# Performance work log

Measured on AMD Instinct MI355X. Metric: run time of the kernel, lower is better.

## Reference

```python
import jax, jax.numpy as jnp
import numpy as np
from jax import lax

B, CIN, COUT, H, W, K = 256, 512, 256, 8, 8, 8192


def setup_inputs() -> dict:
    key = jax.random.key(0)
    ks = jax.random.split(key, 6)
    scale = 0.05
    return {
        "latent": jax.random.normal(ks[0], (B, CIN, H, W), dtype=jnp.float32),
        "conv_w": jax.random.normal(ks[1], (COUT, CIN, 3, 3), dtype=jnp.float32) * scale,
        "conv_b": jax.random.normal(ks[2], (COUT,), dtype=jnp.float32) * scale,
        "lin_w": jax.random.normal(ks[3], (COUT, COUT), dtype=jnp.float32) * scale,
        "lin_b": jax.random.normal(ks[4], (COUT,), dtype=jnp.float32) * scale,
        "emb": jax.random.normal(ks[5], (K, COUT), dtype=jnp.float32),
    }


def reference(latent, conv_w, conv_b, lin_w, lin_b, emb):
    # pre-quantization conv: 3x3, stride 1, padding 1 (SAME), NCHW / OIHW
    x = lax.conv_general_dilated(
        latent, conv_w, window_strides=(1, 1), padding="SAME",
        dimension_numbers=("NCHW", "OIHW", "NCHW"),
    ) + conv_b[None, :, None, None]
    # permute(0,2,3,1) then linear on last dim
    x = jnp.transpose(x, (0, 2, 3, 1))              # [B,H,W,C]
    x = jnp.einsum("bhwc,dc->bhwd", x, lin_w) + lin_b
    flat = x.reshape(-1, x.shape[-1])               # [B*H*W, C]
    distances = (
        jnp.sum(flat ** 2, axis=1, keepdims=True)
        + jnp.sum(emb ** 2, axis=1)
        - 2.0 * flat @ emb.T
    )                                               # [B*H*W, K]
    encoding_indices = jnp.argmin(distances, axis=1)
    return encoding_indices.reshape(-1, 64)
```

## Files before the change

### kernel.cpp

```cpp
#include <hip/hip_runtime.h>
#include <cstdint>
#include <cstddef>


#define CIN_  512
#define E_    4608
#define M_    16384

typedef _Float16 half4_t __attribute__((ext_vector_type(4)));
typedef _Float16 half8_t __attribute__((ext_vector_type(8)));
typedef float f32x4 __attribute__((ext_vector_type(4)));

#define GLOAD_LDS16(gptr, lptr)                                         \
    __builtin_amdgcn_global_load_lds(                                   \
        (const __attribute__((address_space(1))) unsigned int*)(gptr),  \
        (__attribute__((address_space(3))) unsigned int*)(lptr), 16, 0, 0)

__global__ void tkern(const float* __restrict__ src, float* __restrict__ dst,
                      int R, int C) {
    __shared__ float t[32][33];
    int c = blockIdx.x * 32 + threadIdx.x;
    int r = blockIdx.y * 32 + threadIdx.y;
    if (r < R && c < C) t[threadIdx.y][threadIdx.x] = src[(size_t)r * C + c];
    __syncthreads();
    int rr = blockIdx.x * 32 + threadIdx.y;
    int cc = blockIdx.y * 32 + threadIdx.x;
    if (rr < C && cc < R) dst[(size_t)rr * R + cc] = t[threadIdx.x][threadIdx.y];
}

__global__ __launch_bounds__(256) void fold5_k(const float* __restrict__ conv_w,
                                               const float* __restrict__ lwT,
                                               _Float16* __restrict__ W2x) {
    int e0 = blockIdx.x * 8;
    int d = threadIdx.x;
    float acc[8];
    #pragma unroll
    for (int j = 0; j < 8; ++j) acc[j] = 0.f;
    for (int co = 0; co < 256; ++co) {
        float lw = lwT[co * 256 + d];
        const float* cwr = conv_w + (size_t)co * E_ + e0;
        #pragma unroll
        for (int j = 0; j < 8; ++j) acc[j] += cwr[j] * lw;
    }
    #pragma unroll
    for (int j = 0; j < 8; ++j) {
        int e = e0 + j;
        int c = e / 9, t9 = e - c * 9;
        _Float16 h = (_Float16)acc[j];
        _Float16 l = (_Float16)(acc[j] - (float)h);
        W2x[((size_t)(t9 * 256 + d)) * 512 + c] = h;
        W2x[((size_t)((9 + t9) * 256 + d)) * 512 + c] = l;
    }
}

__global__ void bias_k(const float* __restrict__ lwT, const float* __restrict__ conv_b,
                       const float* __restrict__ lin_b, float* __restrict__ b2) {
    int d = threadIdx.x;
    float acc = lin_b[d];
    for (int co = 0; co < 256; ++co) acc += lwT[co * 256 + d] * conv_b[co];
    b2[d] = acc;
}

__global__ __launch_bounds__(256) void packlat_k(const float* __restrict__ lat,
                                                 _Float16* __restrict__ Xnp) {
    int b = blockIdx.x, t = threadIdx.x;
    __shared__ float lt[128][65];
    const float* src = lat + (size_t)b * 512 * 64;
    _Float16* dst = Xnp + (size_t)b * 64 * 1024;
    for (int c0 = 0; c0 < 512; c0 += 128) {
        __syncthreads();
        #pragma unroll
        for (int j = 0; j < 8; ++j) {
            int f4 = t + j * 256;
            int cc = f4 >> 4, p4 = (f4 & 15) * 4;
            float4 v = *(const float4*)(src + (size_t)(c0 + cc) * 64 + p4);
            lt[cc][p4] = v.x; lt[cc][p4 + 1] = v.y;
            lt[cc][p4 + 2] = v.z; lt[cc][p4 + 3] = v.w;
        }
        __syncthreads();
        int pix = t >> 2, cr = (t & 3) * 32;
        #pragma unroll
        for (int q = 0; q < 4; ++q) {
            half8_t hh, ll;
            #pragma unroll
            for (int j = 0; j < 8; ++j) {
                float v = lt[cr + q * 8 + j][pix];
                _Float16 h = (_Float16)v;
                hh[j] = h; ll[j] = (_Float16)(v - (float)h);
            }
            *(half8_t*)(dst + (size_t)pix * 1024 + c0 + cr + q * 8) = hh;
            *(half8_t*)(dst + (size_t)pix * 1024 + 512 + c0 + cr + q * 8) = ll;
        }
    }
}

__global__ __launch_bounds__(256) void convm6_k(
    const _Float16* __restrict__ Xnp, const _Float16* __restrict__ W2x,
    const float* __restrict__ b2, float* __restrict__ yb) {
    __shared__ char sm[65536];
    int m0 = blockIdx.x * 128, n0 = blockIdx.y * 128;
    int tid = threadIdx.x, w = tid >> 6, lane = tid & 63;
    int wm = w & 1, wn = w >> 1;
    int fr = lane & 15, fq = lane >> 4;

    int xq = (fq ^ ((fr >> 1) & 3)) << 4;
    int boff[4];
    #pragma unroll
    for (int i = 0; i < 4; ++i) boff[i] = (wn * 64 + i * 16 + fr) * 64 + xq;
    int imgoff[4], ph[4], pw[4];
    #pragma unroll
    for (int s = 0; s < 4; ++s) {
        int rr = wm * 64 + s * 16 + fr;
        imgoff[s] = rr & 64; ph[s] = (rr >> 3) & 7; pw[s] = rr & 7;
    }
    int slt[2], sr[2], sq[2];
    #pragma unroll
    for (int i = 0; i < 2; ++i) {
        int s = w * 128 + i * 64 + lane;
        slt[i] = s;
        sr[i] = s >> 2;
        sq[i] = ((s & 3) ^ ((s >> 3) & 3)) * 8;
    }

    auto stageA = [&](int cc, int buf) {
        char* L = sm + buf * 16384;
        #pragma unroll
        for (int i = 0; i < 2; ++i) {
            const _Float16* base =
                Xnp + (size_t)(m0 + sr[i]) * 1024 + cc * 32 + sq[i];
            GLOAD_LDS16(base, L + slt[i] * 16);
            GLOAD_LDS16(base + 512, L + 8192 + slt[i] * 16);
        }
    };
    auto stageB = [&](int tap, int cc, int buf) {
        char* L = sm + 32768 + buf * 16384;
        #pragma unroll
        for (int i = 0; i < 2; ++i) {
            const _Float16* bb =
                W2x + ((size_t)(tap * 256 + n0 + sr[i])) * 512 + cc * 32 + sq[i];
            GLOAD_LDS16(bb, L + slt[i] * 16);
            GLOAD_LDS16(bb + (size_t)9 * 256 * 512, L + 8192 + slt[i] * 16);
        }
    };

    f32x4 acc[4][4];
    #pragma unroll
    for (int s = 0; s < 4; ++s)
        #pragma unroll
        for (int t = 0; t < 4; ++t)
            #pragma unroll
            for (int r = 0; r < 4; ++r) acc[s][t][r] = 0.f;

    stageA(0, 0);
    stageB(0, 0, 0);
    const half8_t zfrag = {};
    int gi = 0;
    for (int cc = 0; cc < 16; ++cc) {
        const char* Ab = sm + (cc & 1) * 16384;
        for (int tap = 0; tap < 9; ++tap, ++gi) {
            __syncthreads();
            if (tap < 8) stageB(tap + 1, cc, (gi + 1) & 1);
            else if (cc < 15) stageB(0, cc + 1, (gi + 1) & 1);
            if (tap == 7 && cc < 15) stageA(cc + 1, (cc + 1) & 1);

            int dy = tap / 3 - 1, dx = tap - (tap / 3) * 3 - 1;
            half8_t ah[4], al[4];
            #pragma unroll
            for (int s = 0; s < 4; ++s) {
                int ih = ph[s] + dy, iw = pw[s] + dx;
                bool v = ((unsigned)ih < 8u) && ((unsigned)iw < 8u);
                int pp = imgoff[s] + (v ? ih * 8 + iw : 0);
                int ao = pp * 64 + ((fq ^ ((pp >> 1) & 3)) << 4);
                half8_t a0 = *(const half8_t*)(Ab + ao);
                half8_t a1 = *(const half8_t*)(Ab + 8192 + ao);
                ah[s] = v ? a0 : zfrag;
                al[s] = v ? a1 : zfrag;
            }
            const char* Bb = sm + 32768 + (gi & 1) * 16384;
            half8_t bh[4], bl[4];
            #pragma unroll
            for (int t = 0; t < 4; ++t) {
                bh[t] = *(const half8_t*)(Bb + boff[t]);
                bl[t] = *(const half8_t*)(Bb + 8192 + boff[t]);
            }
            #pragma unroll
            for (int s = 0; s < 4; ++s)
                #pragma unroll
                for (int t = 0; t < 4; ++t)
                    acc[s][t] = __builtin_amdgcn_mfma_f32_16x16x32_f16(
                        ah[s], bh[t], acc[s][t], 0, 0, 0);
            #pragma unroll
            for (int s = 0; s < 4; ++s)
                #pragma unroll
                for (int t = 0; t < 4; ++t)
                    acc[s][t] = __builtin_amdgcn_mfma_f32_16x16x32_f16(
                        ah[s], bl[t], acc[s][t], 0, 0, 0);
            #pragma unroll
            for (int s = 0; s < 4; ++s)
                #pragma unroll
                for (int t = 0; t < 4; ++t)
                    acc[s][t] = __builtin_amdgcn_mfma_f32_16x16x32_f16(
                        al[s], bh[t], acc[s][t], 0, 0, 0);
        }
    }

    float bv[4];
    #pragma unroll
    for (int t = 0; t < 4; ++t) bv[t] = b2[n0 + wn * 64 + t * 16 + fr];
    #pragma unroll
    for (int s = 0; s < 4; ++s)
        #pragma unroll
        for (int r = 0; r < 4; ++r) {
            int m = m0 + wm * 64 + s * 16 + fq * 4 + r;
            #pragma unroll
            for (int t = 0; t < 4; ++t) {
                int d = n0 + wn * 64 + t * 16 + fr;
                yb[(size_t)m * 256 + d] = acc[s][t][r] + bv[t];
            }
        }
}

__global__ __launch_bounds__(256) void pack2_k(
    const float* __restrict__ yb, const float* __restrict__ emb,
    _Float16* __restrict__ A2, _Float16* __restrict__ B2,
    float* __restrict__ esq) {
    #pragma unroll
    for (int it = 0; it < 8; ++it) {
        int i = (blockIdx.x + it * 512) * 256 + threadIdx.x;
        float4 v = *(const float4*)(yb + (size_t)i * 4);
        half4_t h = {(_Float16)v.x, (_Float16)v.y, (_Float16)v.z, (_Float16)v.w};
        *(half4_t*)(A2 + (size_t)i * 4) = h;
    }
    int w = threadIdx.x >> 6, lane = threadIdx.x & 63;
    #pragma unroll
    for (int j = 0; j < 4; ++j) {
        int k = blockIdx.x * 16 + w * 4 + j;
        float4 v = *(const float4*)(emb + (size_t)k * 256 + lane * 4);
        half4_t h = {(_Float16)v.x, (_Float16)v.y, (_Float16)v.z, (_Float16)v.w};
        *(half4_t*)(B2 + (size_t)k * 256 + lane * 4) = h;
        float s = v.x * v.x + v.y * v.y + v.z * v.z + v.w * v.w;
        #pragma unroll
        for (int m = 32; m >= 1; m >>= 1) s += __shfl_xor(s, m, 64);
        if (lane == 0) esq[k] = s;
    }
}

__global__ __launch_bounds__(512) void screen11_k(
    const _Float16* __restrict__ A2, const _Float16* __restrict__ B2,
    const float* __restrict__ esq, float* __restrict__ ps2, int* __restrict__ pi2) {
    __shared__ char sm[49152];
    int Lb = blockIdx.x;
    int xcd = Lb & 7, j = Lb >> 3;
    int mt = xcd * 16 + (j & 15);
    int nt = j >> 4;
    int m0 = mt * 128, n0 = nt * 256;
    int tid = threadIdx.x, w = tid >> 6, lane = tid & 63;
    int wm = w & 1, wn = w >> 1;
    int fr = lane & 15, fq = lane >> 4;

    int xq = (fq ^ ((fr >> 1) & 3)) << 4;
    int aoff[4], boff[4];
    #pragma unroll
    for (int i = 0; i < 4; ++i) {
        aoff[i] = (wm * 64 + i * 16 + fr) * 64 + xq;
        boff[i] = (wn * 64 + i * 16 + fr) * 64 + xq;
    }
    int sAr = tid >> 2, sAq = ((tid & 3) ^ ((tid >> 3) & 3)) * 8;
    int sBs[2], sBr[2], sBq[2];
    #pragma unroll
    for (int i = 0; i < 2; ++i) {
        int s = i * 512 + tid;
        sBs[i] = s;
        sBr[i] = s >> 2;
        sBq[i] = ((s & 3) ^ ((s >> 3) & 3)) * 8;
    }

    auto stage = [&](int kt, int buf) {
        char* L = sm + buf * 24576;
        int ko = kt * 32;
        GLOAD_LDS16(A2 + (size_t)(m0 + sAr) * 256 + ko + sAq, L + tid * 16);
        #pragma unroll
        for (int i = 0; i < 2; ++i)
            GLOAD_LDS16(B2 + (size_t)(n0 + sBr[i]) * 256 + ko + sBq[i],
                        L + 8192 + sBs[i] * 16);
    };

    f32x4 acc[4][4];
    #pragma unroll
    for (int s = 0; s < 4; ++s)
        #pragma unroll
        for (int t = 0; t < 4; ++t)
            #pragma unroll
            for (int r = 0; r < 4; ++r) acc[s][t][r] = 0.f;

    stage(0, 0);
    for (int kt = 0; kt < 8; ++kt) {
        __syncthreads();
        if (kt + 1 < 8) stage(kt + 1, (kt + 1) & 1);
        const char* L = sm + (kt & 1) * 24576;
        half8_t af[4], bf[4];
        #pragma unroll
        for (int s = 0; s < 4; ++s) af[s] = *(const half8_t*)(L + aoff[s]);
        #pragma unroll
        for (int t = 0; t < 4; ++t) bf[t] = *(const half8_t*)(L + 8192 + boff[t]);
        #pragma unroll
        for (int s = 0; s < 4; ++s)
            #pragma unroll
            for (int t = 0; t < 4; ++t)
                acc[s][t] = __builtin_amdgcn_mfma_f32_16x16x32_f16(
                    af[s], bf[t], acc[s][t], 0, 0, 0);
    }

    float esv[4];
    #pragma unroll
    for (int t = 0; t < 4; ++t) esv[t] = esq[n0 + wn * 64 + t * 16 + fr];
    int colIdx = nt * 4 + wn;
    #pragma unroll
    for (int s = 0; s < 4; ++s) {
        #pragma unroll
        for (int r = 0; r < 4; ++r) {
            float best = 3.4e38f; int bidx = 0x7fffffff;
            #pragma unroll
            for (int t = 0; t < 4; ++t) {
                float sc = esv[t] - 2.f * acc[s][t][r];
                int k = n0 + wn * 64 + t * 16 + fr;
                if (sc < best || (sc == best && k < bidx)) { best = sc; bidx = k; }
            }
            #pragma unroll
            for (int msk = 1; msk <= 8; msk <<= 1) {
                float so = __shfl_xor(best, msk, 64);
                int ko2 = __shfl_xor(bidx, msk, 64);
                if (so < best || (so == best && ko2 < bidx)) { best = so; bidx = ko2; }
            }
            if (fr == 0) {
                int m = m0 + wm * 64 + s * 16 + fq * 4 + r;
                ps2[(size_t)m * 128 + colIdx] = best;
                pi2[(size_t)m * 128 + colIdx] = bidx;
            }
        }
    }
}

__global__ __launch_bounds__(256) void refine3_k(
    const float* __restrict__ y, const float* __restrict__ emb,
    const float* __restrict__ esq, const float* __restrict__ ps2,
    const int* __restrict__ pi2, int* __restrict__ out) {
    int lane = threadIdx.x & 63;
    for (int j = 0; j < 8; ++j) {
        int m = blockIdx.x * 32 + j * 4 + (threadIdx.x >> 6);
        float4 yv = *(const float4*)(y + (size_t)m * 256 + lane * 4);
        float sc_[2]; int kc_[2];
        #pragma unroll
        for (int i = 0; i < 2; ++i) {
            sc_[i] = ps2[(size_t)m * 128 + lane * 2 + i];
            kc_[i] = pi2[(size_t)m * 128 + lane * 2 + i];
        }
        float s0 = fminf(sc_[0], sc_[1]);
        #pragma unroll
        for (int msk = 1; msk <= 32; msk <<= 1) s0 = fminf(s0, __shfl_xor(s0, msk, 64));
        float thr = s0 + 0.25f;
        float best = 3.4e38f; int bk = 0x7fffffff;
        for (int c = 0; c < 128; ++c) {
            float scc = __shfl(sc_[c & 1], c >> 1, 64);
            if (scc <= thr) {
                int k = __shfl(kc_[c & 1], c >> 1, 64);
                float4 ev = *(const float4*)(emb + (size_t)k * 256 + lane * 4);
                float d = yv.x * ev.x + yv.y * ev.y + yv.z * ev.z + yv.w * ev.w;
                #pragma unroll
                for (int msk = 1; msk <= 32; msk <<= 1) d += __shfl_xor(d, msk, 64);
                float sx = esq[k] - 2.f * d;
                if (sx < best || (sx == best && k < bk)) { best = sx; bk = k; }
            }
        }
        if (lane == 0) out[m] = bk;
    }
}

extern "C" void kernel_launch(void* const* d_in, const int* in_sizes, int n_in,
                              void* d_out, int out_size, void* d_ws, size_t ws_size,
                              hipStream_t stream) {
    const float* latent = (const float*)d_in[0];
    const float* conv_w = (const float*)d_in[1];
    const float* conv_b = (const float*)d_in[2];
    const float* lin_w  = (const float*)d_in[3];
    const float* lin_b  = (const float*)d_in[4];
    const float* emb    = (const float*)d_in[5];
    int* out = (int*)d_out;

    char* W = (char*)d_ws;
    float*    lwT = (float*)(W + 0);
    float*    b2  = (float*)(W + 262144);
    float*    esq = (float*)(W + 263168);
    float*    yb  = (float*)(W + 295936);
    _Float16* W2x = (_Float16*)(W + 17073152);
    _Float16* Xnp = (_Float16*)(W + 21792768);
    _Float16* A2  = (_Float16*)(W + 21792768);
    _Float16* B2  = (_Float16*)(W + 30181376);
    float*    ps2 = (float*)(W + 34375680);
    int*      pi2 = (int*)(W + 42764288);

    dim3 t32(32, 32);
    tkern<<<dim3(8, 8), t32, 0, stream>>>(lin_w, lwT, 256, 256);
    bias_k<<<1, 256, 0, stream>>>(lwT, conv_b, lin_b, b2);
    fold5_k<<<576, 256, 0, stream>>>(conv_w, lwT, W2x);
    packlat_k<<<256, 256, 0, stream>>>(latent, Xnp);

    convm6_k<<<dim3(128, 2), 256, 0, stream>>>(Xnp, W2x, b2, yb);

    pack2_k<<<512, 256, 0, stream>>>(yb, emb, A2, B2, esq);
    screen11_k<<<4096, 512, 0, stream>>>(A2, B2, esq, ps2, pi2);
    refine3_k<<<512, 256, 0, stream>>>(yb, emb, esq, ps2, pi2, out);
}
```

Measured before the change: 453.2 us.

## Make screening kernel persistent over eight codebook tiles per block

```diff
diff --git a/kernel.cpp b/kernel.cpp
--- a/kernel.cpp
+++ b/kernel.cpp
@@ -245,15 +245,15 @@
     }
 }
 
-__global__ __launch_bounds__(512) void screen11_k(
+__global__ __launch_bounds__(512) void screen12_k(
     const _Float16* __restrict__ A2, const _Float16* __restrict__ B2,
     const float* __restrict__ esq, float* __restrict__ ps2, int* __restrict__ pi2) {
     __shared__ char sm[49152];
-    int Lb = blockIdx.x;
-    int xcd = Lb & 7, j = Lb >> 3;
-    int mt = xcd * 16 + (j & 15);
-    int nt = j >> 4;
-    int m0 = mt * 128, n0 = nt * 256;
+    int b = blockIdx.x;
+    int xcd = b & 7, j0 = b >> 3;
+    int mt = xcd * 16 + (j0 & 15);
+    int m0 = mt * 128;
+    int n0 = (j0 >> 4) * 256;
     int tid = threadIdx.x, w = tid >> 6, lane = tid & 63;
     int wm = w & 1, wn = w >> 1;
     int fr = lane & 15, fq = lane >> 4;
@@ -275,13 +275,13 @@
         sBq[i] = ((s & 3) ^ ((s >> 3) & 3)) * 8;
     }
 
-    auto stage = [&](int kt, int buf) {
+    auto stage = [&](int nn0, int kt, int buf) {
         char* L = sm + buf * 24576;
         int ko = kt * 32;
         GLOAD_LDS16(A2 + (size_t)(m0 + sAr) * 256 + ko + sAq, L + tid * 16);
         #pragma unroll
         for (int i = 0; i < 2; ++i)
-            GLOAD_LDS16(B2 + (size_t)(n0 + sBr[i]) * 256 + ko + sBq[i],
+            GLOAD_LDS16(B2 + (size_t)(nn0 + sBr[i]) * 256 + ko + sBq[i],
                         L + 8192 + sBs[i] * 16);
     };
 
@@ -293,51 +293,62 @@
             #pragma unroll
             for (int r = 0; r < 4; ++r) acc[s][t][r] = 0.f;
 
-    stage(0, 0);
-    for (int kt = 0; kt < 8; ++kt) {
-        __syncthreads();
-        if (kt + 1 < 8) stage(kt + 1, (kt + 1) & 1);
-        const char* L = sm + (kt & 1) * 24576;
-        half8_t af[4], bf[4];
-        #pragma unroll
-        for (int s = 0; s < 4; ++s) af[s] = *(const half8_t*)(L + aoff[s]);
-        #pragma unroll
-        for (int t = 0; t < 4; ++t) bf[t] = *(const half8_t*)(L + 8192 + boff[t]);
+    stage(n0, 0, 0);
+    for (int k8 = 0; k8 < 8; ++k8) {
+        #pragma unroll 1
+        for (int kt = 0; kt < 8; ++kt) {
+            __syncthreads();
+            if (kt < 7)       stage(n0, kt + 1, (kt + 1) & 1);
+            else if (k8 < 7)  stage(n0 + 1024, 0, 0);
+            const char* L = sm + (kt & 1) * 24576;
+            half8_t af[4], bf[4];
+            #pragma unroll
+            for (int s = 0; s < 4; ++s) af[s] = *(const half8_t*)(L + aoff[s]);
+            #pragma unroll
+            for (int t = 0; t < 4; ++t) bf[t] = *(const half8_t*)(L + 8192 + boff[t]);
+            #pragma unroll
+            for (int s = 0; s < 4; ++s)
+                #pragma unroll
+                for (int t = 0; t < 4; ++t)
+                    acc[s][t] = __builtin_amdgcn_mfma_f32_16x16x32_f16(
+                        af[s], bf[t], acc[s][t], 0, 0, 0);
+        }
+
+        float esv[4];
+        #pragma unroll
+        for (int t = 0; t < 4; ++t) esv[t] = esq[n0 + wn * 64 + t * 16 + fr];
+        int colIdx = (n0 >> 6) + wn;
+        #pragma unroll
+        for (int s = 0; s < 4; ++s) {
+            #pragma unroll
+            for (int r = 0; r < 4; ++r) {
+                float best = 3.4e38f; int bidx = 0x7fffffff;
+                #pragma unroll
+                for (int t = 0; t < 4; ++t) {
+                    float sc = esv[t] - 2.f * acc[s][t][r];
+                    int k = n0 + wn * 64 + t * 16 + fr;
+                    if (sc < best || (sc == best && k < bidx)) { best = sc; bidx = k; }
+                }
+                #pragma unroll
+                for (int msk = 1; msk <= 8; msk <<= 1) {
+                    float so = __shfl_xor(best, msk, 64);
+                    int ko2 = __shfl_xor(bidx, msk, 64);
+                    if (so < best || (so == best && ko2 < bidx)) { best = so; bidx = ko2; }
+                }
+                if (fr == 0) {
+                    int m = m0 + wm * 64 + s * 16 + fq * 4 + r;
+                    ps2[(size_t)m * 128 + colIdx] = best;
+                    pi2[(size_t)m * 128 + colIdx] = bidx;
+                }
+            }
+        }
         #pragma unroll
         for (int s = 0; s < 4; ++s)
             #pragma unroll
             for (int t = 0; t < 4; ++t)
-                acc[s][t] = __builtin_amdgcn_mfma_f32_16x16x32_f16(
-                    af[s], bf[t], acc[s][t], 0, 0, 0);
-    }
-
-    float esv[4];
-    #pragma unroll
-    for (int t = 0; t < 4; ++t) esv[t] = esq[n0 + wn * 64 + t * 16 + fr];
-    int colIdx = nt * 4 + wn;
-    #pragma unroll
-    for (int s = 0; s < 4; ++s) {
-        #pragma unroll
-        for (int r = 0; r < 4; ++r) {
-            float best = 3.4e38f; int bidx = 0x7fffffff;
-            #pragma unroll
-            for (int t = 0; t < 4; ++t) {
-                float sc = esv[t] - 2.f * acc[s][t][r];
-                int k = n0 + wn * 64 + t * 16 + fr;
-                if (sc < best || (sc == best && k < bidx)) { best = sc; bidx = k; }
-            }
-            #pragma unroll
-            for (int msk = 1; msk <= 8; msk <<= 1) {
-                float so = __shfl_xor(best, msk, 64);
-                int ko2 = __shfl_xor(bidx, msk, 64);
-                if (so < best || (so == best && ko2 < bidx)) { best = so; bidx = ko2; }
-            }
-            if (fr == 0) {
-                int m = m0 + wm * 64 + s * 16 + fq * 4 + r;
-                ps2[(size_t)m * 128 + colIdx] = best;
-                pi2[(size_t)m * 128 + colIdx] = bidx;
-            }
-        }
+                #pragma unroll
+                for (int r = 0; r < 4; ++r) acc[s][t][r] = 0.f;
+        n0 += 1024;
     }
 }
 
@@ -408,6 +419,6 @@
     convm6_k<<<dim3(128, 2), 256, 0, stream>>>(Xnp, W2x, b2, yb);
 
     pack2_k<<<512, 256, 0, stream>>>(yb, emb, A2, B2, esq);
-    screen11_k<<<4096, 512, 0, stream>>>(A2, B2, esq, ps2, pi2);
+    screen12_k<<<512, 512, 0, stream>>>(A2, B2, esq, ps2, pi2);
     refine3_k<<<512, 256, 0, stream>>>(yb, emb, esq, ps2, pi2, out);
 }
```

Measured after the change: 541.5 us. +19.5%, slower.

## Split conv GEMM reduction over two input-channel halves with fused reduce in pack

Applied to the files above, without the earlier changes.

```diff
diff --git a/kernel.cpp b/kernel.cpp
--- a/kernel.cpp
+++ b/kernel.cpp
@@ -94,11 +94,13 @@
     }
 }
 
-__global__ __launch_bounds__(256) void convm6_k(
+__global__ __launch_bounds__(256) void convm8_k(
     const _Float16* __restrict__ Xnp, const _Float16* __restrict__ W2x,
-    const float* __restrict__ b2, float* __restrict__ yb) {
+    const float* __restrict__ b2, float* __restrict__ yb,
+    float* __restrict__ tmp) {
     __shared__ char sm[65536];
     int m0 = blockIdx.x * 128, n0 = blockIdx.y * 128;
+    int cc0 = blockIdx.z * 8;
     int tid = threadIdx.x, w = tid >> 6, lane = tid & 63;
     int wm = w & 1, wn = w >> 1;
     int fr = lane & 15, fq = lane >> 4;
@@ -151,17 +153,18 @@
             #pragma unroll
             for (int r = 0; r < 4; ++r) acc[s][t][r] = 0.f;
 
-    stageA(0, 0);
-    stageB(0, 0, 0);
+    stageA(cc0, 0);
+    stageB(0, cc0, 0);
     const half8_t zfrag = {};
     int gi = 0;
-    for (int cc = 0; cc < 16; ++cc) {
-        const char* Ab = sm + (cc & 1) * 16384;
+    for (int cci = 0; cci < 8; ++cci) {
+        int cc = cc0 + cci;
+        const char* Ab = sm + (cci & 1) * 16384;
         for (int tap = 0; tap < 9; ++tap, ++gi) {
             __syncthreads();
             if (tap < 8) stageB(tap + 1, cc, (gi + 1) & 1);
-            else if (cc < 15) stageB(0, cc + 1, (gi + 1) & 1);
-            if (tap == 7 && cc < 15) stageA(cc + 1, (cc + 1) & 1);
+            else if (cci < 7) stageB(0, cc + 1, (gi + 1) & 1);
+            if (tap == 7 && cci < 7) stageA(cc + 1, (cci + 1) & 1);
 
             int dy = tap / 3 - 1, dx = tap - (tap / 3) * 3 - 1;
             half8_t ah[4], al[4];
@@ -204,9 +207,11 @@
         }
     }
 
+    float* dst = (blockIdx.z == 0) ? yb : tmp;
     float bv[4];
     #pragma unroll
-    for (int t = 0; t < 4; ++t) bv[t] = b2[n0 + wn * 64 + t * 16 + fr];
+    for (int t = 0; t < 4; ++t)
+        bv[t] = (blockIdx.z == 0) ? b2[n0 + wn * 64 + t * 16 + fr] : 0.f;
     #pragma unroll
     for (int s = 0; s < 4; ++s)
         #pragma unroll
@@ -215,20 +220,24 @@
             #pragma unroll
             for (int t = 0; t < 4; ++t) {
                 int d = n0 + wn * 64 + t * 16 + fr;
-                yb[(size_t)m * 256 + d] = acc[s][t][r] + bv[t];
-            }
-        }
-}
-
-__global__ __launch_bounds__(256) void pack2_k(
-    const float* __restrict__ yb, const float* __restrict__ emb,
+                dst[(size_t)m * 256 + d] = acc[s][t][r] + bv[t];
+            }
+        }
+}
+
+__global__ __launch_bounds__(256) void pack3_k(
+    float* __restrict__ yb, const float* __restrict__ tmp,
+    const float* __restrict__ emb,
     _Float16* __restrict__ A2, _Float16* __restrict__ B2,
     float* __restrict__ esq) {
     #pragma unroll
     for (int it = 0; it < 8; ++it) {
         int i = (blockIdx.x + it * 512) * 256 + threadIdx.x;
         float4 v = *(const float4*)(yb + (size_t)i * 4);
-        half4_t h = {(_Float16)v.x, (_Float16)v.y, (_Float16)v.z, (_Float16)v.w};
+        float4 t = *(const float4*)(tmp + (size_t)i * 4);
+        float4 s = {v.x + t.x, v.y + t.y, v.z + t.z, v.w + t.w};
+        *(float4*)(yb + (size_t)i * 4) = s;
+        half4_t h = {(_Float16)s.x, (_Float16)s.y, (_Float16)s.z, (_Float16)s.w};
         *(half4_t*)(A2 + (size_t)i * 4) = h;
     }
     int w = threadIdx.x >> 6, lane = threadIdx.x & 63;
@@ -398,6 +407,7 @@
     _Float16* B2  = (_Float16*)(W + 30181376);
     float*    ps2 = (float*)(W + 34375680);
     int*      pi2 = (int*)(W + 42764288);
+    float*    tmp = (float*)(W + 34375680);
 
     dim3 t32(32, 32);
     tkern<<<dim3(8, 8), t32, 0, stream>>>(lin_w, lwT, 256, 256);
@@ -405,9 +415,9 @@
     fold5_k<<<576, 256, 0, stream>>>(conv_w, lwT, W2x);
     packlat_k<<<256, 256, 0, stream>>>(latent, Xnp);
 
-    convm6_k<<<dim3(128, 2), 256, 0, stream>>>(Xnp, W2x, b2, yb);
-
-    pack2_k<<<512, 256, 0, stream>>>(yb, emb, A2, B2, esq);
+    convm8_k<<<dim3(128, 2, 2), 256, 0, stream>>>(Xnp, W2x, b2, yb, tmp);
+
+    pack3_k<<<512, 256, 0, stream>>>(yb, tmp, emb, A2, B2, esq);
     screen11_k<<<4096, 512, 0, stream>>>(A2, B2, esq, ps2, pi2);
     refine3_k<<<512, 256, 0, stream>>>(yb, emb, esq, ps2, pi2, out);
 }
```

Measured after the change: 474.9 us. 1.05x slower.
